# Kernel tuning notes

Hardware: AMD Instinct MI355X
Metric: run time of the kernel (lower is better)

Reference implementation:

```python
import jax, jax.numpy as jnp
import numpy as np

B, S, D = 4, 2048, 512
H, DK, DV = 8, 64, 64

def setup_inputs() -> dict:
    key = jax.random.key(0)
    ks = jax.random.split(key, 11)
    s = 0.02
    return {
        "q_in": jax.random.normal(ks[0], (B, S, D), jnp.float32),
        "k_in": jax.random.normal(ks[1], (B, S, D), jnp.float32),
        "v_in": jax.random.normal(ks[2], (B, S, D), jnp.float32),
        "Wq": jax.random.normal(ks[3], (H, D, DK), jnp.float32) * s,
        "bq": jax.random.normal(ks[4], (H, DK), jnp.float32) * s,
        "Wk": jax.random.normal(ks[5], (H, D, DK), jnp.float32) * s,
        "bk": jax.random.normal(ks[6], (H, DK), jnp.float32) * s,
        "Wv": jax.random.normal(ks[7], (H, D, DV), jnp.float32) * s,
        "bv": jax.random.normal(ks[8], (H, DV), jnp.float32) * s,
        "Wo": jax.random.normal(ks[9], (H * DV, D), jnp.float32) * s,
        "bo": jax.random.normal(ks[10], (D,), jnp.float32) * s,
    }


def reference(q_in, k_in, v_in, Wq, bq, Wk, bk, Wv, bv, Wo, bo):
    # Per-head Q/K/V projections, batched over heads (same math as the
    # original Python loop over SingleAttention heads).
    q = jnp.einsum("bsd,hdk->bhsk", q_in, Wq) + bq[None, :, None, :]   # [B,H,S,DK]
    k = jnp.einsum("bsd,hdk->bhsk", k_in, Wk) + bk[None, :, None, :]   # [B,H,S,DK]
    v = jnp.einsum("bsd,hdv->bhsv", v_in, Wv) + bv[None, :, None, :]   # [B,H,S,DV]
    scale = 1.0 / jnp.sqrt(jnp.float32(DK))
    scores = jnp.einsum("bhqk,bhsk->bhqs", q, k) * scale               # [B,H,S,S]
    attn = jax.nn.softmax(scores, axis=-1)
    out = jnp.einsum("bhqs,bhsv->bhqv", attn, v)                        # [B,H,S,DV]
    # concat heads along feature dim: [B,S,H*DV]
    concat = out.transpose(0, 2, 1, 3).reshape(B, S, H * DV)
    return concat @ Wo + bo                                             # [B,S,D]
```

## Files before the change

### kernel.cpp

```cpp
#include <hip/hip_runtime.h>
#include <hip/hip_bf16.h>

using bf16 = __hip_bfloat16;
typedef short short8  __attribute__((ext_vector_type(8)));
typedef short short4v __attribute__((ext_vector_type(4)));
typedef float float4v __attribute__((ext_vector_type(4)));
typedef float f32x16  __attribute__((ext_vector_type(16)));
typedef unsigned int uint4v __attribute__((ext_vector_type(4)));

#define MFMA_BF16   __builtin_amdgcn_mfma_f32_16x16x32_bf16
#define MFMA32_BF16 __builtin_amdgcn_mfma_f32_32x32x16_bf16

#define B_  4
#define S_  2048
#define D_  512
#define H_  8
#define DK_ 64

__device__ __forceinline__ short f2bf(float f) {
  bf16 h = __float2bfloat16(f);
  return *reinterpret_cast<short*>(&h);
}

__device__ __forceinline__ unsigned cvtpk(float lo, float hi) {
  unsigned r;
  asm("v_cvt_pk_bf16_f32 %0, %1, %2" : "=v"(r) : "v"(lo), "v"(hi));
  return r;
}

__device__ __forceinline__ void plswap(unsigned& a, unsigned& b) {
  asm("v_permlane32_swap_b32 %0, %1" : "+v"(a), "+v"(b));
}

__device__ __forceinline__ short8 mk8(unsigned v0, unsigned v1, unsigned v2,
                                      unsigned v3) {
  uint4v u;
  u[0] = v0; u[1] = v1; u[2] = v2; u[3] = v3;
  return __builtin_bit_cast(short8, u);
}

#define GLL(g, l) __builtin_amdgcn_global_load_lds(                        \
      (const __attribute__((address_space(1))) void*)(g),                  \
      (__attribute__((address_space(3))) void*)(l), 16, 0, 0)

__global__ __launch_bounds__(256)
void prep(const float* __restrict__ qin, const float* __restrict__ kin,
          const float* __restrict__ vin, short* __restrict__ Xb,
          const float* __restrict__ Wq, const float* __restrict__ Wk,
          const float* __restrict__ Wv, const float* __restrict__ Wo,
          short* __restrict__ WqT, short* __restrict__ WkT,
          short* __restrict__ WvT, short* __restrict__ WoT) {
  __shared__ float tile[64 * 65];
  const int bid = blockIdx.x, tid = threadIdx.x;
  const size_t NTOK = (size_t)B_ * S_ * D_;

  if (bid < 6144) {
    const int z = bid >> 11, blk = bid & 2047;
    const float* src = (z == 0) ? qin : (z == 1) ? kin : vin;
    short* dst = Xb + (size_t)z * NTOK;
    const size_t base = ((size_t)blk * 256 + tid) * 8;
    float4v f0 = *(const float4v*)&src[base];
    float4v f1 = *(const float4v*)&src[base + 4];
    short8 s;
#pragma unroll
    for (int j = 0; j < 4; j++) { s[j] = f2bf(f0[j]); s[j + 4] = f2bf(f1[j]); }
    *(short8*)&dst[base] = s;
    return;
  }

  const int tw = bid - 6144;
  const int mat = tw >> 6, t = tw & 63;
  const float* W = (mat == 0) ? Wq : (mat == 1) ? Wk : (mat == 2) ? Wv : Wo;
  short* T       = (mat == 0) ? WqT : (mat == 1) ? WkT : (mat == 2) ? WvT : WoT;

  size_t sbase, ss, dbase;
  if (mat < 3) {
    int hh = t >> 3, d0 = (t & 7) * 64;
    sbase = (size_t)hh * 32768 + (size_t)d0 * 64;
    ss = 64;
    dbase = (size_t)hh * 64 * 512 + d0;
  } else {
    int n0 = (t >> 3) * 64, k0 = (t & 7) * 64;
    sbase = (size_t)k0 * 512 + n0;
    ss = 512;
    dbase = (size_t)n0 * 512 + k0;
  }

  {
    int r = tid >> 2, c0 = (tid & 3) * 16;
#pragma unroll
    for (int j = 0; j < 4; j++)
      *(float4v*)&tile[r * 65 + c0 + j * 4] =
          *(const float4v*)&W[sbase + (size_t)r * ss + c0 + j * 4];
  }
  __syncthreads();
  {
    int c = tid >> 2, r0 = (tid & 3) * 16;
#pragma unroll
    for (int j = 0; j < 2; j++) {
      short8 s;
#pragma unroll
      for (int u = 0; u < 8; u++) s[u] = f2bf(tile[(r0 + j * 8 + u) * 65 + c]);
      *(short8*)&T[dbase + (size_t)c * 512 + r0 + j * 8] = s;
    }
  }
}

__device__ __forceinline__ void gemm_core2(const short* __restrict__ A,
                                           const short* __restrict__ Bt,
                                           int m0, int n0,
                                           short* As, short* Bs,
                                           float4v acc[4][4]) {
  const int tid  = threadIdx.x;
  const int lane = tid & 63, wave = tid >> 6;
  const int quad = lane >> 4, l16 = lane & 15;
  const int wm = (wave >> 1) * 64, wn = (wave & 1) * 64;

  for (int k0 = 0; k0 < 512; k0 += 64) {
    __syncthreads();
#pragma unroll
    for (int i = 0; i < 4; i++) {
      int s = wave * 256 + i * 64 + lane;
      int row = s >> 3, cs = s & 7;
      int gc = (cs ^ (row & 7)) << 3;
      GLL(&A[(size_t)(m0 + row) * 512 + k0 + gc],
          &As[(size_t)(wave * 256 + i * 64) * 8]);
      GLL(&Bt[(size_t)(n0 + row) * 512 + k0 + gc],
          &Bs[(size_t)(wave * 256 + i * 64) * 8]);
    }
    __syncthreads();
#pragma unroll
    for (int ks = 0; ks < 64; ks += 32) {
      const int sr = (ks >> 3) + quad;
      short8 af[4], bfr[4];
#pragma unroll
      for (int mi = 0; mi < 4; mi++) {
        int row = wm + mi * 16 + l16;
        af[mi] = *(short8*)&As[row * 64 + ((sr ^ (row & 7)) << 3)];
      }
#pragma unroll
      for (int ni = 0; ni < 4; ni++) {
        int row = wn + ni * 16 + l16;
        bfr[ni] = *(short8*)&Bs[row * 64 + ((sr ^ (row & 7)) << 3)];
      }
#pragma unroll
      for (int mi = 0; mi < 4; mi++)
#pragma unroll
        for (int ni = 0; ni < 4; ni++)
          acc[mi][ni] = MFMA_BF16(af[mi], bfr[ni], acc[mi][ni], 0, 0, 0);
    }
  }
}

__global__ __launch_bounds__(256, 2)
void qkv_gemm(const short* __restrict__ Xb,
              const short* __restrict__ WqT, const short* __restrict__ WkT,
              const short* __restrict__ WvT,
              const float* __restrict__ bq, const float* __restrict__ bk,
              const float* __restrict__ bv,
              short* __restrict__ Qp, short* __restrict__ Kp,
              short* __restrict__ Vt) {
  __shared__ __align__(16) short As[128 * 64];
  __shared__ __align__(16) short Bs[128 * 64];
  const int m0 = blockIdx.x * 128, n0 = blockIdx.y * 128;
  const int z = blockIdx.z;
  const size_t NTOK = (size_t)B_ * S_ * D_;
  const short* A    = Xb + (size_t)z * NTOK;
  const short* Bt   = (z == 0) ? WqT : (z == 1) ? WkT : WvT;
  const float* bias = (z == 0) ? bq  : (z == 1) ? bk  : bv;
  const float scale = (z == 0) ? 0.125f * 1.44269504088896f : 1.0f;

  float4v acc[4][4];
#pragma unroll
  for (int mi = 0; mi < 4; mi++)
#pragma unroll
    for (int ni = 0; ni < 4; ni++) acc[mi][ni] = (float4v){0.f, 0.f, 0.f, 0.f};

  gemm_core2(A, Bt, m0, n0, As, Bs, acc);

  const int lane = threadIdx.x & 63, wave = threadIdx.x >> 6;
  const int quad = lane >> 4, l16 = lane & 15;
  const int wm = (wave >> 1) * 64, wn = (wave & 1) * 64;

  if (z < 2) {
    short* out = (z == 0) ? Qp : Kp;
#pragma unroll
    for (int mi = 0; mi < 4; mi++) {
      int m = m0 + wm + mi * 16 + quad * 4;
      int b = m >> 11, s = m & 2047;
#pragma unroll
      for (int ni = 0; ni < 4; ni++) {
        int n = n0 + wn + ni * 16 + l16;
        int h = n >> 6, dk = n & 63;
        float bb = bias[n];
        size_t base = (((size_t)b * H_ + h) * S_ + s) * 64 + dk;
#pragma unroll
        for (int r = 0; r < 4; r++)
          out[base + (size_t)r * 64] = f2bf((acc[mi][ni][r] + bb) * scale);
      }
    }
  } else {
#pragma unroll
    for (int mi = 0; mi < 4; mi++) {
      int m = m0 + wm + mi * 16 + quad * 4;
      int b = m >> 11, s = m & 2047;
#pragma unroll
      for (int ni = 0; ni < 4; ni++) {
        int n = n0 + wn + ni * 16 + l16;
        int h = n >> 6, v = n & 63;
        float bb = bias[n];
        short4v pk;
#pragma unroll
        for (int r = 0; r < 4; r++) pk[r] = f2bf(acc[mi][ni][r] + bb);
        *(short4v*)&Vt[(((size_t)b * H_ + h) * 64 + v) * S_ + s] = pk;
      }
    }
  }
}

__global__ __launch_bounds__(512, 4)
void attn_kernel(const short* __restrict__ Qp, const short* __restrict__ Kp,
                 const short* __restrict__ Vt, short* __restrict__ Ao) {
  __shared__ __align__(16) short sh[32768];

  const int orig = blockIdx.y * gridDim.x + blockIdx.x;
  const int lb = (orig & 7) * 64 + (orig >> 3);
  const int qt = lb & 15, bh = lb >> 4;
  const int b = bh >> 3, h = bh & 7;

  const int tid = threadIdx.x;
  const int lane = tid & 63, wave = tid >> 6;
  const int wg = wave & 3, half = wave >> 2;
  const int l31 = lane & 31, hi = lane >> 5, s7 = l31 & 7;

  const short* Qb = Qp + (size_t)bh * S_ * 64;
  const short* Kb = Kp + (size_t)bh * S_ * 64 + (size_t)half * 1024 * 64;
  const short* Vb = Vt + (size_t)bh * 64 * S_;

  short8 qf[4];
  {
    const short* qrow = Qb + (size_t)(qt * 128 + wg * 32 + l31) * 64;
#pragma unroll
    for (int w = 0; w < 4; w++)
      qf[w] = *(const short8*)&qrow[w * 16 + hi * 8];
  }

  const int slot0 = wg * 128 + lane;
  const int kr0 = slot0 >> 3, kc0 = slot0 & 7;
  const int kr1 = kr0 + 8;
  const short* kg0 = Kb + (size_t)kr0 * 64 + ((kc0 ^ (kr0 & 7)) << 3);
  const short* kg1 = Kb + (size_t)kr1 * 64 + ((kc0 ^ (kr1 & 7)) << 3);
  const short* vg0 = Vb + (size_t)kr0 * S_ + half * 1024 + ((kc0 ^ (kr0 & 7)) << 3);
  const short* vg1 = Vb + (size_t)kr1 * S_ + half * 1024 + ((kc0 ^ (kr1 & 7)) << 3);

  short* Kbase = sh;
  short* Vbase = sh + 16384;

  f32x16 acc0, acc1;
#pragma unroll
  for (int r = 0; r < 16; r++) { acc0[r] = 0.f; acc1[r] = 0.f; }
  float ls0 = 0.f, ls1 = 0.f;

  {
    short* kd = Kbase + (half * 2) * 4096 + wg * 1024;
    short* vd = Vbase + (half * 2) * 4096 + wg * 1024;
    GLL(kg0, kd); GLL(kg1, kd + 512);
    GLL(vg0, vd); GLL(vg1, vd + 512);
  }
  __syncthreads();

  for (int t = 0; t < 16; t++) {
    const int cur = t & 1;
    if (t < 15) {
      short* kd = Kbase + (half * 2 + (cur ^ 1)) * 4096 + wg * 1024;
      short* vd = Vbase + (half * 2 + (cur ^ 1)) * 4096 + wg * 1024;
      GLL(kg0 + (size_t)(t + 1) * 4096, kd);
      GLL(kg1 + (size_t)(t + 1) * 4096, kd + 512);
      GLL(vg0 + (size_t)(t + 1) * 64, vd);
      GLL(vg1 + (size_t)(t + 1) * 64, vd + 512);
    }
    const short* kb = Kbase + (half * 2 + cur) * 4096;
    const short* vs = Vbase + (half * 2 + cur) * 4096;

#pragma unroll
    for (int kt = 0; kt < 2; kt++) {
      f32x16 sa;
#pragma unroll
      for (int r = 0; r < 16; r++) sa[r] = 0.f;
      __builtin_amdgcn_s_setprio(1);
#pragma unroll
      for (int w = 0; w < 4; w++) {
        short8 kf = *(const short8*)&kb[(kt * 32 + l31) * 64 +
                                        (((2 * w + hi) ^ s7) << 3)];
        sa = MFMA32_BF16(kf, qf[w], sa, 0, 0, 0);
      }
      __builtin_amdgcn_s_setprio(0);

      float pv[16];
#pragma unroll
      for (int r = 0; r < 16; r++) pv[r] = exp2f(sa[r]);
#pragma unroll
      for (int r = 0; r < 8; r++) { ls0 += pv[r]; ls1 += pv[r + 8]; }

      unsigned a0 = cvtpk(pv[0], pv[1]),  b0 = cvtpk(pv[4], pv[5]);
      plswap(a0, b0);
      unsigned c0 = cvtpk(pv[2], pv[3]),  d0 = cvtpk(pv[6], pv[7]);
      plswap(c0, d0);
      short8 pa0 = mk8(a0, c0, b0, d0);
      unsigned a1 = cvtpk(pv[8], pv[9]),  b1 = cvtpk(pv[12], pv[13]);
      plswap(a1, b1);
      unsigned c1 = cvtpk(pv[10], pv[11]), d1 = cvtpk(pv[14], pv[15]);
      plswap(c1, d1);
      short8 pa1 = mk8(a1, c1, b1, d1);

      __builtin_amdgcn_s_setprio(1);
      {
        const int kw0 = kt * 2, kw1 = kt * 2 + 1;
        short8 v00 = *(const short8*)&vs[l31 * 64 + (((2 * kw0 + hi) ^ s7) << 3)];
        short8 v10 = *(const short8*)&vs[(32 + l31) * 64 + (((2 * kw0 + hi) ^ s7) << 3)];
        acc0 = MFMA32_BF16(pa0, v00, acc0, 0, 0, 0);
        acc1 = MFMA32_BF16(pa0, v10, acc1, 0, 0, 0);
        short8 v01 = *(const short8*)&vs[l31 * 64 + (((2 * kw1 + hi) ^ s7) << 3)];
        short8 v11 = *(const short8*)&vs[(32 + l31) * 64 + (((2 * kw1 + hi) ^ s7) << 3)];
        acc0 = MFMA32_BF16(pa1, v01, acc0, 0, 0, 0);
        acc1 = MFMA32_BF16(pa1, v11, acc1, 0, 0, 0);
      }
      __builtin_amdgcn_s_setprio(0);
    }
    __syncthreads();
  }

  float lsum = ls0 + ls1;
  lsum += __shfl_xor(lsum, 32, 64);

  float* fsh = (float*)sh;
  if (half == 1) {
    const int base = wg * 2304 + lane * 36;
#pragma unroll
    for (int r = 0; r < 16; r += 4) {
      *(float4v*)&fsh[base + r] =
          (float4v){acc0[r], acc0[r + 1], acc0[r + 2], acc0[r + 3]};
      *(float4v*)&fsh[base + 16 + r] =
          (float4v){acc1[r], acc1[r + 1], acc1[r + 2], acc1[r + 3]};
    }
    if (lane < 32) fsh[9216 + wg * 32 + l31] = lsum;
  }
  __syncthreads();
  if (half == 1) return;

  {
    const int base = wg * 2304 + lane * 36;
#pragma unroll
    for (int r = 0; r < 16; r += 4) {
      float4v u0 = *(float4v*)&fsh[base + r];
      acc0[r] += u0[0]; acc0[r + 1] += u0[1];
      acc0[r + 2] += u0[2]; acc0[r + 3] += u0[3];
      float4v u1 = *(float4v*)&fsh[base + 16 + r];
      acc1[r] += u1[0]; acc1[r + 1] += u1[1];
      acc1[r + 2] += u1[2]; acc1[r + 3] += u1[3];
    }
    lsum += fsh[9216 + wg * 32 + l31];
  }
  float myrl = 1.0f / lsum;

  const size_t obase =
      ((size_t)b * S_ + (size_t)(qt * 128 + wg * 32)) * D_ + h * 64 + l31;
#pragma unroll
  for (int r = 0; r < 16; r++) {
    int q = (r & 3) + 8 * (r >> 2) + 4 * hi;
    float rl = __shfl(myrl, q, 64);
    Ao[obase + (size_t)q * D_]      = f2bf(acc0[r] * rl);
    Ao[obase + (size_t)q * D_ + 32] = f2bf(acc1[r] * rl);
  }
}

__global__ __launch_bounds__(256, 2)
void out_gemm(const short* __restrict__ A, const short* __restrict__ Bt,
              const float* __restrict__ bias, float* __restrict__ out) {
  __shared__ __align__(16) short As[128 * 64];
  __shared__ __align__(16) short Bs[128 * 64];
  const int m0 = blockIdx.x * 128, n0 = blockIdx.y * 128;

  float4v acc[4][4];
#pragma unroll
  for (int mi = 0; mi < 4; mi++)
#pragma unroll
    for (int ni = 0; ni < 4; ni++) acc[mi][ni] = (float4v){0.f, 0.f, 0.f, 0.f};

  gemm_core2(A, Bt, m0, n0, As, Bs, acc);

  const int lane = threadIdx.x & 63, wave = threadIdx.x >> 6;
  const int quad = lane >> 4, l16 = lane & 15;
  const int wm = (wave >> 1) * 64, wn = (wave & 1) * 64;
#pragma unroll
  for (int mi = 0; mi < 4; mi++) {
    int m = m0 + wm + mi * 16 + quad * 4;
#pragma unroll
    for (int ni = 0; ni < 4; ni++) {
      int n = n0 + wn + ni * 16 + l16;
      float bb = bias[n];
#pragma unroll
      for (int r = 0; r < 4; r++)
        out[(size_t)(m + r) * 512 + n] = acc[mi][ni][r] + bb;
    }
  }
}

extern "C" void kernel_launch(void* const* d_in, const int* in_sizes, int n_in,
                              void* d_out, int out_size, void* d_ws, size_t ws_size,
                              hipStream_t stream) {
  const float* qin = (const float*)d_in[0];
  const float* kin = (const float*)d_in[1];
  const float* vin = (const float*)d_in[2];
  const float* Wq  = (const float*)d_in[3];
  const float* bq  = (const float*)d_in[4];
  const float* Wk  = (const float*)d_in[5];
  const float* bk  = (const float*)d_in[6];
  const float* Wv  = (const float*)d_in[7];
  const float* bv  = (const float*)d_in[8];
  const float* Wo  = (const float*)d_in[9];
  const float* bo  = (const float*)d_in[10];
  float* out = (float*)d_out;
  short* ws  = (short*)d_ws;

  const size_t NTOK = (size_t)B_ * S_ * D_;
  short* Qp  = ws;
  short* Kp  = ws + NTOK;
  short* Vt  = ws + 2 * NTOK;
  short* Ao  = ws + 3 * NTOK;
  short* WqT = ws + 4 * NTOK;
  short* WkT = WqT + 512 * 512;
  short* WvT = WkT + 512 * 512;
  short* WoT = WvT + 512 * 512;
  short* Xb  = WoT + 512 * 512;

  prep<<<dim3(6400), 256, 0, stream>>>(qin, kin, vin, Xb, Wq, Wk, Wv, Wo,
                                       WqT, WkT, WvT, WoT);
  qkv_gemm<<<dim3(64, 4, 3), 256, 0, stream>>>(Xb, WqT, WkT, WvT,
                                               bq, bk, bv, Qp, Kp, Vt);
  attn_kernel<<<dim3(16, 32), 512, 0, stream>>>(Qp, Kp, Vt, Ao);
  out_gemm<<<dim3(64, 4), 256, 0, stream>>>(Ao, WoT, bo, out);
}
```

Baseline: 196.5 us.

## Double-buffer LDS tiles in projection GEMMs to overlap loads with MFMA

The shared GEMM core used by the QKV projection and output projection kernels now keeps two LDS buffers for the A and B tiles. It issues the global-to-LDS load of the next K slice before computing on the current one, so memory latency can overlap with MFMA work. The cost is twice the LDS per block (64 KB), which may reduce blocks per CU, plus explicit vmcnt waits and barriers.

```diff
diff --git a/kernel.cpp b/kernel.cpp
--- a/kernel.cpp
+++ b/kernel.cpp
@@ -116,19 +116,19 @@
   const int quad = lane >> 4, l16 = lane & 15;
   const int wm = (wave >> 1) * 64, wn = (wave & 1) * 64;
 
-  for (int k0 = 0; k0 < 512; k0 += 64) {
-    __syncthreads();
+  auto stage = [&](int buf, int k0) {
 #pragma unroll
     for (int i = 0; i < 4; i++) {
-      int s = wave * 256 + i * 64 + lane;
-      int row = s >> 3, cs = s & 7;
+      int sl = wave * 256 + i * 64 + lane;
+      int row = sl >> 3, cs = sl & 7;
       int gc = (cs ^ (row & 7)) << 3;
       GLL(&A[(size_t)(m0 + row) * 512 + k0 + gc],
-          &As[(size_t)(wave * 256 + i * 64) * 8]);
+          &As[buf * 8192 + (wave * 256 + i * 64) * 8]);
       GLL(&Bt[(size_t)(n0 + row) * 512 + k0 + gc],
-          &Bs[(size_t)(wave * 256 + i * 64) * 8]);
-    }
-    __syncthreads();
+          &Bs[buf * 8192 + (wave * 256 + i * 64) * 8]);
+    }
+  };
+  auto comp = [&](int buf) {
 #pragma unroll
     for (int ks = 0; ks < 64; ks += 32) {
       const int sr = (ks >> 3) + quad;
@@ -136,12 +136,12 @@
 #pragma unroll
       for (int mi = 0; mi < 4; mi++) {
         int row = wm + mi * 16 + l16;
-        af[mi] = *(short8*)&As[row * 64 + ((sr ^ (row & 7)) << 3)];
+        af[mi] = *(short8*)&As[buf * 8192 + row * 64 + ((sr ^ (row & 7)) << 3)];
       }
 #pragma unroll
       for (int ni = 0; ni < 4; ni++) {
         int row = wn + ni * 16 + l16;
-        bfr[ni] = *(short8*)&Bs[row * 64 + ((sr ^ (row & 7)) << 3)];
+        bfr[ni] = *(short8*)&Bs[buf * 8192 + row * 64 + ((sr ^ (row & 7)) << 3)];
       }
 #pragma unroll
       for (int mi = 0; mi < 4; mi++)
@@ -149,6 +149,21 @@
         for (int ni = 0; ni < 4; ni++)
           acc[mi][ni] = MFMA_BF16(af[mi], bfr[ni], acc[mi][ni], 0, 0, 0);
     }
+  };
+
+  stage(0, 0);
+  asm volatile("s_waitcnt vmcnt(0)" ::: "memory");
+  __syncthreads();
+#pragma unroll
+  for (int k0 = 0; k0 < 512; k0 += 128) {
+    stage(1, k0 + 64);
+    comp(0);
+    asm volatile("s_waitcnt vmcnt(0)" ::: "memory");
+    __syncthreads();
+    if (k0 + 128 < 512) stage(0, k0 + 128);
+    comp(1);
+    asm volatile("s_waitcnt vmcnt(0)" ::: "memory");
+    __syncthreads();
   }
 }
 
@@ -160,8 +175,8 @@
               const float* __restrict__ bv,
               short* __restrict__ Qp, short* __restrict__ Kp,
               short* __restrict__ Vt) {
-  __shared__ __align__(16) short As[128 * 64];
-  __shared__ __align__(16) short Bs[128 * 64];
+  __shared__ __align__(16) short As[2 * 128 * 64];
+  __shared__ __align__(16) short Bs[2 * 128 * 64];
   const int m0 = blockIdx.x * 128, n0 = blockIdx.y * 128;
   const int z = blockIdx.z;
   const size_t NTOK = (size_t)B_ * S_ * D_;
@@ -377,8 +392,8 @@
 __global__ __launch_bounds__(256, 2)
 void out_gemm(const short* __restrict__ A, const short* __restrict__ Bt,
               const float* __restrict__ bias, float* __restrict__ out) {
-  __shared__ __align__(16) short As[128 * 64];
-  __shared__ __align__(16) short Bs[128 * 64];
+  __shared__ __align__(16) short As[2 * 128 * 64];
+  __shared__ __align__(16) short Bs[2 * 128 * 64];
   const int m0 = blockIdx.x * 128, n0 = blockIdx.y * 128;
 
   float4v acc[4][4];
```

Result: no change. 196.4 us (-0.1%).
